# Performance work log

Measured on AMD Instinct MI355X. Metric: run time of the kernel, lower is better.

The kernel has to match this reference:

```python
import jax, jax.numpy as jnp
import numpy as np


def _pairwise_sq_dist(x, y):
    # x: [B, N, 3], y: [B, M, 3] -> P: [B, N, M] squared Euclidean distances
    xx = jnp.sum(x * x, axis=-1)                      # [B, N]
    yy = jnp.sum(y * y, axis=-1)                      # [B, M]
    zz = jnp.einsum('bnd,bmd->bnm', x, y)             # [B, N, M]
    return xx[:, :, None] + yy[:, None, :] - 2.0 * zz


def setup_inputs() -> dict:
    key = jax.random.key(0)
    k1, k2 = jax.random.split(key)
    B, K = 8, 8192
    adv_pc = jax.random.normal(k1, (B, K, 3), dtype=jnp.float32)
    ori_pc = jax.random.normal(k2, (B, K, 3), dtype=jnp.float32)
    weights = jnp.ones((B,), dtype=jnp.float32)
    return {"adv_pc": adv_pc, "ori_pc": ori_pc, "weights": weights}


def reference(adv_pc, ori_pc, weights):
    # P = pairwise_dist(gts=ori_pc, preds=adv_pc): [B, N_ori, N_adv]
    P = _pairwise_sq_dist(ori_pc, adv_pc)
    # method='adv2ori': loss1 = max over adv points of min over ori points
    loss1 = jnp.max(jnp.min(P, axis=1), axis=1)       # [B]
    loss = loss1 * weights
    return jnp.mean(loss)                             # batch_avg=True
```

## Files before the change

### kernel.cpp

```cpp
#include <hip/hip_runtime.h>


#define KPTS 8192
#define BATCH 8

#define CBLK 256
#define NSPLIT 8
#define RBLK (KPTS / NSPLIT)
#define CHUNK 256
#define NCHUNK (RBLK / CHUNK)
#define CTILES (CHUNK / 32)

typedef _Float16 half8 __attribute__((ext_vector_type(8)));
typedef float f32x16 __attribute__((ext_vector_type(16)));

__device__ __forceinline__ float min16(const f32x16 c) {
    float u0 = fminf(fminf(c[0],  c[1]),  c[2]);
    float u1 = fminf(fminf(c[3],  c[4]),  c[5]);
    float u2 = fminf(fminf(c[6],  c[7]),  c[8]);
    float u3 = fminf(fminf(c[9],  c[10]), c[11]);
    float u4 = fminf(fminf(c[12], c[13]), c[14]);
    float u5 = fminf(fminf(u0, u1), c[15]);
    float u6 = fminf(fminf(u2, u3), u4);
    return fminf(u5, u6);
}

__device__ __forceinline__ void mk_afrag(float x, float y, float z,
                                         half8& a0, half8& a1) {
    const _Float16 Z = (_Float16)0.0f;
    float oo = x * x + y * y + z * z;
    _Float16 hx = (_Float16)x, hy = (_Float16)y, hz = (_Float16)z;
    _Float16 lx = (_Float16)(x - (float)hx);
    _Float16 ly = (_Float16)(y - (float)hy);
    _Float16 lz = (_Float16)(z - (float)hz);
    _Float16 oh = (_Float16)oo;
    _Float16 ol = (_Float16)(oo - (float)oh);
    a0 = half8{hx, hy, hz, hx, hy, hz, lx, ly};
    a1 = half8{lz, oh, ol, Z, Z, Z, Z, Z};
}

__global__ __launch_bounds__(256) void hausdorff(const float* __restrict__ adv,
                                                 const float* __restrict__ ori,
                                                 float* __restrict__ part,
                                                 float* __restrict__ out) {
    __shared__ _Float16 sA[2][CHUNK * 16];

    const int bid  = blockIdx.x;
    const int b    = bid >> 8;
    const int mc   = (bid >> 3) & 31;
    const int ns   = bid & 7;
    const int tid  = threadIdx.x;
    const int lane = tid & 63;
    const int wv   = tid >> 6;
    const int r    = lane & 31;
    const int hk   = lane >> 5;

    if (bid == 0 && tid == 0) out[0] = 0.0f;

    const _Float16 Z = (_Float16)0.0f, ONE = (_Float16)1.0f;

    const float* advb = adv + (size_t)b * KPTS * 3;
    const int m0 = mc * CBLK + wv * 64 + r;
    const int m1 = m0 + 32;
    half8 bf0, bf1;
    float aa0, aa1;
    {
        float ax = advb[3 * m0], ay = advb[3 * m0 + 1], az = advb[3 * m0 + 2];
        aa0 = ax * ax + ay * ay + az * az;
        float tx = -2.f * ax, ty = -2.f * ay, tz = -2.f * az;
        _Float16 bx = (_Float16)tx, by = (_Float16)ty, bz = (_Float16)tz;
        _Float16 cx = (_Float16)(tx - (float)bx);
        _Float16 cy = (_Float16)(ty - (float)by);
        _Float16 cz = (_Float16)(tz - (float)bz);
        half8 h0 = {bx, by, bz, cx, cy, cz, bx, by};
        half8 h1 = {bz, ONE, ONE, Z, Z, Z, Z, Z};
        bf0 = hk ? h1 : h0;
    }
    {
        float ax = advb[3 * m1], ay = advb[3 * m1 + 1], az = advb[3 * m1 + 2];
        aa1 = ax * ax + ay * ay + az * az;
        float tx = -2.f * ax, ty = -2.f * ay, tz = -2.f * az;
        _Float16 bx = (_Float16)tx, by = (_Float16)ty, bz = (_Float16)tz;
        _Float16 cx = (_Float16)(tx - (float)bx);
        _Float16 cy = (_Float16)(ty - (float)by);
        _Float16 cz = (_Float16)(tz - (float)bz);
        half8 h0 = {bx, by, bz, cx, cy, cz, bx, by};
        half8 h1 = {bz, ONE, ONE, Z, Z, Z, Z, Z};
        bf1 = hk ? h1 : h0;
    }

    f32x16 zc;
#pragma unroll
    for (int i = 0; i < 16; ++i) zc[i] = 0.0f;

    float rm0 = __builtin_huge_valf();
    float rm1 = __builtin_huge_valf();

    const float* orib = ori + (size_t)b * KPTS * 3;
    const int rowbase = ns * RBLK;

    const int woff = ((tid >> 5) << 9) + ((tid & 31) << 3);

    {
        const float* op = orib + (size_t)(rowbase + tid) * 3;
        half8 a0, a1;
        mk_afrag(op[0], op[1], op[2], a0, a1);
        *(half8*)(&sA[0][woff])       = a0;
        *(half8*)(&sA[0][woff + 256]) = a1;
    }
    __syncthreads();

    const int roff = lane << 3;

    for (int ch = 0; ch < NCHUNK; ++ch) {
        const int cur = ch & 1;

        float px, py, pz;
        if (ch + 1 < NCHUNK) {
            const float* op = orib + (size_t)(rowbase + (ch + 1) * CHUNK + tid) * 3;
            px = op[0]; py = op[1]; pz = op[2];
        }

        const _Float16* apl = &sA[cur][roff];
#pragma unroll 4
        for (int t = 0; t < CTILES; ++t) {
            half8 af = *(const half8*)(apl + (size_t)t * 512);
            f32x16 c0 = __builtin_amdgcn_mfma_f32_32x32x16_f16(af, bf0, zc, 0, 0, 0);
            f32x16 c1 = __builtin_amdgcn_mfma_f32_32x32x16_f16(af, bf1, zc, 0, 0, 0);
            rm0 = fminf(rm0, min16(c0));
            rm1 = fminf(rm1, min16(c1));
        }

        if (ch + 1 < NCHUNK) {
            half8 a0, a1;
            mk_afrag(px, py, pz, a0, a1);
            *(half8*)(&sA[cur ^ 1][woff])       = a0;
            *(half8*)(&sA[cur ^ 1][woff + 256]) = a1;
            __syncthreads();
        }
    }

    rm0 = fminf(rm0, __shfl_xor(rm0, 32, 64));
    rm1 = fminf(rm1, __shfl_xor(rm1, 32, 64));

    float v0 = fmaxf(rm0 + aa0, 0.0f);
    float v1 = fmaxf(rm1 + aa1, 0.0f);

    float* p = part + ((size_t)ns * BATCH + b) * KPTS;
    if (hk == 0) {
        p[m0] = v0;
        p[m1] = v1;
    }
}

__global__ __launch_bounds__(1024) void reduceB(const float* __restrict__ part,
                                                const float* __restrict__ w,
                                                float* __restrict__ out) {
    const int b = blockIdx.x;
    const int tid = threadIdx.x;

    float mx = 0.0f;
#pragma unroll
    for (int h = 0; h < 2; ++h) {
        const int c4 = tid + h * 1024;
        float4 v[NSPLIT];
#pragma unroll
        for (int s = 0; s < NSPLIT; ++s)
            v[s] = *(const float4*)(part + ((size_t)s * BATCH + b) * KPTS + (size_t)c4 * 4);
        float4 mn = v[0];
#pragma unroll
        for (int s = 1; s < NSPLIT; ++s) {
            mn.x = fminf(mn.x, v[s].x); mn.y = fminf(mn.y, v[s].y);
            mn.z = fminf(mn.z, v[s].z); mn.w = fminf(mn.w, v[s].w);
        }
        mx = fmaxf(mx, fmaxf(fmaxf(mn.x, mn.y), fmaxf(mn.z, mn.w)));
    }

#pragma unroll
    for (int off = 32; off; off >>= 1)
        mx = fmaxf(mx, __shfl_xor(mx, off, 64));

    __shared__ float red[16];
    if ((tid & 63) == 0) red[tid >> 6] = mx;
    __syncthreads();
    if (tid == 0) {
        float m2 = red[0];
#pragma unroll
        for (int i = 1; i < 16; ++i) m2 = fmaxf(m2, red[i]);
        atomicAdd(out, m2 * w[b] * (1.0f / BATCH));
    }
}

extern "C" void kernel_launch(void* const* d_in, const int* in_sizes, int n_in,
                              void* d_out, int out_size, void* d_ws, size_t ws_size,
                              hipStream_t stream) {
    const float* adv = (const float*)d_in[0];
    const float* ori = (const float*)d_in[1];
    const float* w   = (const float*)d_in[2];
    float* out = (float*)d_out;
    float* part = (float*)d_ws;

    hausdorff<<<BATCH * 32 * NSPLIT, 256, 0, stream>>>(adv, ori, part, out);
    reduceB<<<BATCH, 1024, 0, stream>>>((const float*)part, w, out);
}
```

Measured before the change: 85.22 us.

## Precompute ori MFMA fragments in a prep kernel and widen per-wave column tiles

A new prep kernel converts the ori points once into split-fp16 MFMA A-fragments in global workspace, laid out in tile order. The main kernel then streams those fragments straight from global memory into registers with a one-step software prefetch, dropping the shared-memory double buffer, the barriers, and the conversion that every column block used to repeat. Each wave now handles four 32-column adv tiles instead of two, so each loaded A fragment feeds four MFMAs and the grid is halved. The cost is an extra kernel launch, more global/L2 traffic for the fragments, and higher register pressure. The prefetch also reads one tile past the slice end, which stays inside the workspace only because of the padding before the partials buffer.

```diff
diff --git a/kernel.cpp b/kernel.cpp
--- a/kernel.cpp
+++ b/kernel.cpp
@@ -3,18 +3,17 @@
 
 #define KPTS 8192
 #define BATCH 8
-
-#define CBLK 256
 #define NSPLIT 8
 #define RBLK (KPTS / NSPLIT)
-#define CHUNK 256
-#define NCHUNK (RBLK / CHUNK)
-#define CTILES (CHUNK / 32)
+#define TSLICE (RBLK / 32)
+#define CBLK 512
+#define MCHUNK (KPTS / CBLK)
+#define AHALF_B (KPTS * 16)
 
 typedef _Float16 half8 __attribute__((ext_vector_type(8)));
 typedef float f32x16 __attribute__((ext_vector_type(16)));
 
-__device__ __forceinline__ float min16(const f32x16 c) {
+__device__ __forceinline__ float min16acc(float rm, const f32x16 c) {
     float u0 = fminf(fminf(c[0],  c[1]),  c[2]);
     float u1 = fminf(fminf(c[3],  c[4]),  c[5]);
     float u2 = fminf(fminf(c[6],  c[7]),  c[8]);
@@ -22,32 +21,40 @@
     float u4 = fminf(fminf(c[12], c[13]), c[14]);
     float u5 = fminf(fminf(u0, u1), c[15]);
     float u6 = fminf(fminf(u2, u3), u4);
-    return fminf(u5, u6);
+    return fminf(fminf(u5, u6), rm);
 }
 
-__device__ __forceinline__ void mk_afrag(float x, float y, float z,
-                                         half8& a0, half8& a1) {
+__global__ __launch_bounds__(256) void prep(const float* __restrict__ ori,
+                                            _Float16* __restrict__ Ap) {
+    const int g = blockIdx.x * 256 + threadIdx.x;
+    const int b = g >> 13;
+    const int n = g & (KPTS - 1);
+
+    const float* op = ori + (size_t)g * 3;
+    float x = op[0], y = op[1], z = op[2];
+    float oo = x * x + y * y + z * z;
     const _Float16 Z = (_Float16)0.0f;
-    float oo = x * x + y * y + z * z;
     _Float16 hx = (_Float16)x, hy = (_Float16)y, hz = (_Float16)z;
     _Float16 lx = (_Float16)(x - (float)hx);
     _Float16 ly = (_Float16)(y - (float)hy);
     _Float16 lz = (_Float16)(z - (float)hz);
     _Float16 oh = (_Float16)oo;
     _Float16 ol = (_Float16)(oo - (float)oh);
-    a0 = half8{hx, hy, hz, hx, hy, hz, lx, ly};
-    a1 = half8{lz, oh, ol, Z, Z, Z, Z, Z};
+    half8 a0 = {hx, hy, hz, hx, hy, hz, lx, ly};
+    half8 a1 = {lz, oh, ol, Z, Z, Z, Z, Z};
+
+    _Float16* base = Ap + (size_t)b * AHALF_B + ((n >> 5) << 9) + ((n & 31) << 3);
+    *(half8*)base         = a0;
+    *(half8*)(base + 256) = a1;
 }
 
 __global__ __launch_bounds__(256) void hausdorff(const float* __restrict__ adv,
-                                                 const float* __restrict__ ori,
+                                                 const _Float16* __restrict__ Ap,
                                                  float* __restrict__ part,
                                                  float* __restrict__ out) {
-    __shared__ _Float16 sA[2][CHUNK * 16];
-
     const int bid  = blockIdx.x;
-    const int b    = bid >> 8;
-    const int mc   = (bid >> 3) & 31;
+    const int b    = bid >> 7;
+    const int mc   = (bid >> 3) & (MCHUNK - 1);
     const int ns   = bid & 7;
     const int tid  = threadIdx.x;
     const int lane = tid & 63;
@@ -60,13 +67,14 @@
     const _Float16 Z = (_Float16)0.0f, ONE = (_Float16)1.0f;
 
     const float* advb = adv + (size_t)b * KPTS * 3;
-    const int m0 = mc * CBLK + wv * 64 + r;
-    const int m1 = m0 + 32;
-    half8 bf0, bf1;
-    float aa0, aa1;
-    {
-        float ax = advb[3 * m0], ay = advb[3 * m0 + 1], az = advb[3 * m0 + 2];
-        aa0 = ax * ax + ay * ay + az * az;
+    const int m0 = mc * CBLK + wv * 128 + r;
+    half8 bf0, bf1, bf2, bf3;
+    float aa0, aa1, aa2, aa3;
+#pragma unroll
+    for (int i = 0; i < 4; ++i) {
+        const int m = m0 + 32 * i;
+        float ax = advb[3 * m], ay = advb[3 * m + 1], az = advb[3 * m + 2];
+        float aa = ax * ax + ay * ay + az * az;
         float tx = -2.f * ax, ty = -2.f * ay, tz = -2.f * az;
         _Float16 bx = (_Float16)tx, by = (_Float16)ty, bz = (_Float16)tz;
         _Float16 cx = (_Float16)(tx - (float)bx);
@@ -74,82 +82,49 @@
         _Float16 cz = (_Float16)(tz - (float)bz);
         half8 h0 = {bx, by, bz, cx, cy, cz, bx, by};
         half8 h1 = {bz, ONE, ONE, Z, Z, Z, Z, Z};
-        bf0 = hk ? h1 : h0;
-    }
-    {
-        float ax = advb[3 * m1], ay = advb[3 * m1 + 1], az = advb[3 * m1 + 2];
-        aa1 = ax * ax + ay * ay + az * az;
-        float tx = -2.f * ax, ty = -2.f * ay, tz = -2.f * az;
-        _Float16 bx = (_Float16)tx, by = (_Float16)ty, bz = (_Float16)tz;
-        _Float16 cx = (_Float16)(tx - (float)bx);
-        _Float16 cy = (_Float16)(ty - (float)by);
-        _Float16 cz = (_Float16)(tz - (float)bz);
-        half8 h0 = {bx, by, bz, cx, cy, cz, bx, by};
-        half8 h1 = {bz, ONE, ONE, Z, Z, Z, Z, Z};
-        bf1 = hk ? h1 : h0;
+        half8 bi = hk ? h1 : h0;
+        if (i == 0) { bf0 = bi; aa0 = aa; }
+        else if (i == 1) { bf1 = bi; aa1 = aa; }
+        else if (i == 2) { bf2 = bi; aa2 = aa; }
+        else { bf3 = bi; aa3 = aa; }
     }
 
     f32x16 zc;
 #pragma unroll
     for (int i = 0; i < 16; ++i) zc[i] = 0.0f;
 
-    float rm0 = __builtin_huge_valf();
-    float rm1 = __builtin_huge_valf();
+    float rm0 = __builtin_huge_valf(), rm1 = __builtin_huge_valf();
+    float rm2 = __builtin_huge_valf(), rm3 = __builtin_huge_valf();
 
-    const float* orib = ori + (size_t)b * KPTS * 3;
-    const int rowbase = ns * RBLK;
+    const half8* __restrict__ ap =
+        (const half8*)(Ap + (size_t)b * AHALF_B + (size_t)ns * TSLICE * 512) + lane;
 
-    const int woff = ((tid >> 5) << 9) + ((tid & 31) << 3);
-
-    {
-        const float* op = orib + (size_t)(rowbase + tid) * 3;
-        half8 a0, a1;
-        mk_afrag(op[0], op[1], op[2], a0, a1);
-        *(half8*)(&sA[0][woff])       = a0;
-        *(half8*)(&sA[0][woff + 256]) = a1;
-    }
-    __syncthreads();
-
-    const int roff = lane << 3;
-
-    for (int ch = 0; ch < NCHUNK; ++ch) {
-        const int cur = ch & 1;
-
-        float px, py, pz;
-        if (ch + 1 < NCHUNK) {
-            const float* op = orib + (size_t)(rowbase + (ch + 1) * CHUNK + tid) * 3;
-            px = op[0]; py = op[1]; pz = op[2];
-        }
-
-        const _Float16* apl = &sA[cur][roff];
+    half8 af = ap[0];
 #pragma unroll 4
-        for (int t = 0; t < CTILES; ++t) {
-            half8 af = *(const half8*)(apl + (size_t)t * 512);
-            f32x16 c0 = __builtin_amdgcn_mfma_f32_32x32x16_f16(af, bf0, zc, 0, 0, 0);
-            f32x16 c1 = __builtin_amdgcn_mfma_f32_32x32x16_f16(af, bf1, zc, 0, 0, 0);
-            rm0 = fminf(rm0, min16(c0));
-            rm1 = fminf(rm1, min16(c1));
-        }
-
-        if (ch + 1 < NCHUNK) {
-            half8 a0, a1;
-            mk_afrag(px, py, pz, a0, a1);
-            *(half8*)(&sA[cur ^ 1][woff])       = a0;
-            *(half8*)(&sA[cur ^ 1][woff + 256]) = a1;
-            __syncthreads();
-        }
+    for (int t = 0; t < TSLICE; ++t) {
+        half8 afn = ap[(t + 1) * 64];
+        f32x16 c0 = __builtin_amdgcn_mfma_f32_32x32x16_f16(af, bf0, zc, 0, 0, 0);
+        f32x16 c1 = __builtin_amdgcn_mfma_f32_32x32x16_f16(af, bf1, zc, 0, 0, 0);
+        f32x16 c2 = __builtin_amdgcn_mfma_f32_32x32x16_f16(af, bf2, zc, 0, 0, 0);
+        f32x16 c3 = __builtin_amdgcn_mfma_f32_32x32x16_f16(af, bf3, zc, 0, 0, 0);
+        rm0 = min16acc(rm0, c0);
+        rm1 = min16acc(rm1, c1);
+        rm2 = min16acc(rm2, c2);
+        rm3 = min16acc(rm3, c3);
+        af = afn;
     }
 
     rm0 = fminf(rm0, __shfl_xor(rm0, 32, 64));
     rm1 = fminf(rm1, __shfl_xor(rm1, 32, 64));
-
-    float v0 = fmaxf(rm0 + aa0, 0.0f);
-    float v1 = fmaxf(rm1 + aa1, 0.0f);
+    rm2 = fminf(rm2, __shfl_xor(rm2, 32, 64));
+    rm3 = fminf(rm3, __shfl_xor(rm3, 32, 64));
 
     float* p = part + ((size_t)ns * BATCH + b) * KPTS;
     if (hk == 0) {
-        p[m0] = v0;
-        p[m1] = v1;
+        p[m0]      = fmaxf(rm0 + aa0, 0.0f);
+        p[m0 + 32] = fmaxf(rm1 + aa1, 0.0f);
+        p[m0 + 64] = fmaxf(rm2 + aa2, 0.0f);
+        p[m0 + 96] = fmaxf(rm3 + aa3, 0.0f);
     }
 }
 
@@ -198,8 +173,12 @@
     const float* ori = (const float*)d_in[1];
     const float* w   = (const float*)d_in[2];
     float* out = (float*)d_out;
-    float* part = (float*)d_ws;
 
-    hausdorff<<<BATCH * 32 * NSPLIT, 256, 0, stream>>>(adv, ori, part, out);
+    char* ws = (char*)d_ws;
+    _Float16* Ap = (_Float16*)ws;
+    float* part = (float*)(ws + (size_t)(2 << 20) + 4096);
+
+    prep<<<(BATCH * KPTS) / 256, 256, 0, stream>>>(ori, Ap);
+    hausdorff<<<BATCH * MCHUNK * NSPLIT, 256, 0, stream>>>(adv, (const _Float16*)Ap, part, out);
     reduceB<<<BATCH, 1024, 0, stream>>>((const float*)part, w, out);
 }
```

New measurement: 89.17 us. 4.6% more time.
